# Kernel tuning notes

Measured on AMD Instinct MI355X. Metric: run time of the kernel, lower is better.

## Reference

```python
import jax, jax.numpy as jnp
import numpy as np

ALPHA = 0.2  # leaky_relu negative slope
NEG_INF = -9e15


def gat_layer(h_in, W, a, adj_mask):
    """One GATLayer (eval mode, dropout disabled).
    h_in: [N, F_in], W: [F_in, F_out], a: [2*F_out, 1], adj_mask: [N, N] bool.
    Equivalent to the torch repeat/cat construction: e_ij = leaky_relu(a1.h_i + a2.h_j).
    """
    h = h_in @ W                          # [N, F_out]
    F_out = W.shape[1]
    a1 = a[:F_out, 0]                     # [F_out]
    a2 = a[F_out:, 0]                     # [F_out]
    f1 = h @ a1                           # [N]
    f2 = h @ a2                           # [N]
    e = jax.nn.leaky_relu(f1[:, None] + f2[None, :], negative_slope=ALPHA)  # [N, N]
    e = jnp.where(adj_mask, e, NEG_INF)
    attn = jax.nn.softmax(e, axis=-1)     # rows sum to 1
    return jax.nn.elu(attn @ h)           # [N, F_out]


def setup_inputs() -> dict:
    key = jax.random.key(0)
    ks = jax.random.split(key, 6)
    N, F_in, F_hid, F_out, H = 8192, 29, 8, 2, 4
    x = jax.random.normal(ks[0], (N, F_in), dtype=jnp.float32)
    adj = jax.random.randint(ks[1], (N, N), 0, 2, dtype=jnp.int32)
    # xavier_uniform with gain=1.414
    def xavier(k, shape, gain=1.414):
        fan_in, fan_out = shape[0], shape[1]
        bound = gain * np.sqrt(6.0 / (fan_in + fan_out))
        return jax.random.uniform(k, shape, jnp.float32, -bound, bound)
    W_heads = jnp.stack([xavier(k, (F_in, F_hid)) for k in jax.random.split(ks[2], H)])   # [H, 29, 8]
    a_heads = jnp.stack([xavier(k, (2 * F_hid, 1)) for k in jax.random.split(ks[3], H)])  # [H, 16, 1]
    W_out = xavier(ks[4], (F_hid * H, F_out))   # [32, 2]
    a_out = xavier(ks[5], (2 * F_out, 1))       # [4, 1]
    return {"x": x, "adj": adj, "W_heads": W_heads, "a_heads": a_heads,
            "W_out": W_out, "a_out": a_out}


def reference(x, adj, W_heads, a_heads, W_out, a_out):
    adj_mask = adj > 0
    heads = jax.vmap(lambda W, a: gat_layer(x, W, a, adj_mask))(W_heads, a_heads)  # [H, N, 8]
    hcat = jnp.concatenate(list(heads), axis=1)   # [N, H*8] (same order as torch cat over heads)
    out = gat_layer(hcat, W_out, a_out, adj_mask)  # [N, 2]
    return jax.nn.log_softmax(out, axis=1)
```

## Files before the change

### kernel.cpp

```cpp
#include <hip/hip_runtime.h>
#include <math.h>

#define N 8192
#define FIN 29
#define FH 8
#define NH 4
#define ALPHA 0.2f
#define LOG2E 1.4426950408889634f
#define JS 8
#define JRR (N / JS)

typedef unsigned long long ull;
typedef unsigned short u16;
typedef __attribute__((ext_vector_type(8))) short bf16x8;
typedef __attribute__((ext_vector_type(4))) float f32x4;
typedef __attribute__((ext_vector_type(2))) float f32x2;

__device__ inline unsigned bf16rn(float f) {
    unsigned u = __float_as_uint(f);
    return (u + 0x7fffu + ((u >> 16) & 1u)) >> 16;
}
__device__ inline f32x2 pk_mul(f32x2 a, f32x2 b) {
    f32x2 d;
    asm("v_pk_mul_f32 %0, %1, %2" : "=v"(d) : "v"(a), "v"(b));
    return d;
}

#define WTILE(E1P2, E1N2, SW, ACC)                                              \
    {                                                                           \
        f32x2 wp, wn;                                                           \
        float w0, w1, w2, w3, w4, w5, w6, w7;                                   \
        wp = pk_mul(E1P2, p01); wn = pk_mul(E1N2, n01);                         \
        w0 = fmaxf(wp[0], wn[0]); w1 = fmaxf(wp[1], wn[1]);                     \
        wp = pk_mul(E1P2, p23); wn = pk_mul(E1N2, n23);                         \
        w2 = fmaxf(wp[0], wn[0]); w3 = fmaxf(wp[1], wn[1]);                     \
        wp = pk_mul(E1P2, p45); wn = pk_mul(E1N2, n45);                         \
        w4 = fmaxf(wp[0], wn[0]); w5 = fmaxf(wp[1], wn[1]);                     \
        wp = pk_mul(E1P2, p67); wn = pk_mul(E1N2, n67);                         \
        w6 = fmaxf(wp[0], wn[0]); w7 = fmaxf(wp[1], wn[1]);                     \
        w0 = (SW & 1u)   ? w0 : 0.f;                                            \
        w1 = (SW & 2u)   ? w1 : 0.f;                                            \
        w2 = (SW & 4u)   ? w2 : 0.f;                                            \
        w3 = (SW & 8u)   ? w3 : 0.f;                                            \
        w4 = (SW & 16u)  ? w4 : 0.f;                                            \
        w5 = (SW & 32u)  ? w5 : 0.f;                                            \
        w6 = (SW & 64u)  ? w6 : 0.f;                                            \
        w7 = (SW & 128u) ? w7 : 0.f;                                            \
        uint4 ap;                                                               \
        asm("v_cvt_pk_bf16_f32 %0, %1, %2" : "=v"(ap.x) : "v"(w0), "v"(w1));    \
        asm("v_cvt_pk_bf16_f32 %0, %1, %2" : "=v"(ap.y) : "v"(w2), "v"(w3));    \
        asm("v_cvt_pk_bf16_f32 %0, %1, %2" : "=v"(ap.z) : "v"(w4), "v"(w5));    \
        asm("v_cvt_pk_bf16_f32 %0, %1, %2" : "=v"(ap.w) : "v"(w6), "v"(w7));    \
        ACC = __builtin_amdgcn_mfma_f32_16x16x32_bf16(                          \
            __builtin_bit_cast(bf16x8, ap), __builtin_bit_cast(bf16x8, bp),     \
            ACC, 0, 0, 0);                                                      \
    }

__global__ void kPack(const int* __restrict__ adj, ull* __restrict__ maskT) {
    int row = blockIdx.x;
    int tid = threadIdx.x;
    int lane = tid & 63;
    int wv = tid >> 6;
    const int* rp = adj + (size_t)row * N;
#pragma unroll 8
    for (int i = 0; i < 32; i++) {
        int a = rp[i * 256 + tid];
        ull b = __ballot(a > 0);
        if (lane == 0) maskT[(size_t)(i * 4 + wv) * N + row] = b;
    }
}

__global__ __launch_bounds__(256) void kFeat(
    const float* __restrict__ x, const float* __restrict__ Wh,
    const float* __restrict__ ah,
    float* __restrict__ e2p, float* __restrict__ e2n, u16* __restrict__ Bpk,
    float* __restrict__ f1a, float* __restrict__ bmax1) {
    __shared__ float sx[64 * FIN];
    __shared__ float sW[NH * FIN * FH];
    __shared__ float sa[NH * 2 * FH];
    int tid = threadIdx.x;
    int wv = tid >> 6;
    for (int i = tid; i < NH * FIN * FH; i += 256) sW[i] = Wh[i];
    for (int i = tid; i < NH * 2 * FH; i += 256) sa[i] = ah[i];
    for (int i = tid; i < 64 * FIN; i += 256) sx[i] = x[(size_t)blockIdx.x * 64 * FIN + i];
    __syncthreads();
    int h = tid & 3;
    int nl = tid >> 2;
    int node = blockIdx.x * 64 + nl;
    float hv[FH];
#pragma unroll
    for (int k = 0; k < FH; k++) {
        float s = 0.f;
#pragma unroll
        for (int f = 0; f < FIN; f++) s += sx[nl * FIN + f] * sW[(h * FIN + f) * FH + k];
        hv[k] = s;
    }
    float f1 = 0.f, f2 = 0.f;
#pragma unroll
    for (int k = 0; k < FH; k++) {
        f1 += hv[k] * sa[h * 16 + k];
        f2 += hv[k] * sa[h * 16 + 8 + k];
    }
    float f1L = f1 * LOG2E, f2L = f2 * LOG2E;
    f1a[node * 4 + h] = f1L;
    e2p[(size_t)h * N + node] = __builtin_amdgcn_exp2f(f2L);
    e2n[(size_t)h * N + node] = __builtin_amdgcn_exp2f(ALPHA * f2L);
    int js = (node >> 10) & 7;
    int t  = (node >> 6) & 15;
    int hfl = (node >> 5) & 1;
    int kb = (node >> 3) & 3;
    int e  = node & 7;
    u16* dst = Bpk + ((size_t)(((h * 8 + js) * 16 + t) * 2 + hfl)) * 512 + e;
#pragma unroll
    for (int cc = 0; cc < 16; cc++) {
        u16 vv = (cc < FH) ? (u16)bf16rn(hv[cc])
                           : ((cc == 8) ? (u16)0x3F80u : (u16)0);
        dst[(kb * 16 + cc) * 8] = vv;
    }
    float v = f2L;
    for (int off = 4; off < 64; off <<= 1) v = fmaxf(v, __shfl_xor(v, off, 64));
    if ((tid & 63) < 4) bmax1[(tid & 3) * 512 + blockIdx.x * 4 + wv] = v;
}

__global__ __launch_bounds__(256, 6) void kB_attn1(
    const ull* __restrict__ maskT, const float* __restrict__ e2p,
    const float* __restrict__ e2n, const uint4* __restrict__ Bpk,
    const float* __restrict__ f1a, const float* __restrict__ bmax1,
    float* __restrict__ part1) {
    __shared__ __align__(16) float sE2p[JRR];
    __shared__ __align__(16) float sE2n[JRR];
    __shared__ float sred[4];
    int tid = threadIdx.x;
    int lane = tid & 63;
    int wv = tid >> 6;
    int h = blockIdx.x & 3;
    int js = (blockIdx.x >> 2) & 7;
    int rowblk = blockIdx.x >> 5;
    int jbase = js * JRR;

#pragma unroll
    for (int i = 0; i < JRR / 256; i++) {
        sE2p[tid + i * 256] = e2p[(size_t)h * N + jbase + tid + i * 256];
        sE2n[tid + i * 256] = e2n[(size_t)h * N + jbase + tid + i * 256];
    }
    float v = -3.0e38f;
    for (int i = tid; i < 512; i += 256) v = fmaxf(v, bmax1[h * 512 + i]);
    for (int off = 32; off > 0; off >>= 1) v = fmaxf(v, __shfl_xor(v, off, 64));
    if (lane == 0) sred[wv] = v;
    __syncthreads();
    float mfL = fmaxf(fmaxf(sred[0], sred[1]), fmaxf(sred[2], sred[3]));

    int c = lane & 15;
    int kb = lane >> 4;
    int sh = kb * 8;
    int r0 = rowblk * 128 + wv * 16 + c;
    int r1 = r0 + 64;

    float f1 = f1a[r0 * 4 + h];
    float vv = f1 + mfL, mm = fmaxf(vv, ALPHA * vv);
    f32x2 e1p0, e1n0, e1p1, e1n1;
    e1p0[0] = e1p0[1] = __builtin_amdgcn_exp2f(f1 - mm);
    e1n0[0] = e1n0[1] = __builtin_amdgcn_exp2f(ALPHA * f1 - mm);
    f1 = f1a[r1 * 4 + h];
    vv = f1 + mfL; mm = fmaxf(vv, ALPHA * vv);
    e1p1[0] = e1p1[1] = __builtin_amdgcn_exp2f(f1 - mm);
    e1n1[0] = e1n1[1] = __builtin_amdgcn_exp2f(ALPHA * f1 - mm);

    const ull* mT = maskT + (size_t)(js * (JRR / 64)) * N;
    const uint4* bp0 = Bpk + (size_t)(h * 8 + js) * 2048 + lane;
    const float* pph = sE2p + kb * 8;
    const float* nnh = sE2n + kb * 8;

    f32x4 acc0 = {0.f, 0.f, 0.f, 0.f};
    f32x4 acc1 = {0.f, 0.f, 0.f, 0.f};

    for (int t = 0; t < JRR / 64; t++) {
        ull mw0 = mT[(size_t)t * N + r0];
        ull mw1 = mT[(size_t)t * N + r1];
#pragma unroll
        for (int hf = 0; hf < 2; hf++) {
            f32x4 P0 = *(const f32x4*)(pph + t * 64 + hf * 32);
            f32x4 P1 = *(const f32x4*)(pph + t * 64 + hf * 32 + 4);
            f32x4 Q0 = *(const f32x4*)(nnh + t * 64 + hf * 32);
            f32x4 Q1 = *(const f32x4*)(nnh + t * 64 + hf * 32 + 4);
            f32x2 p01 = __builtin_shufflevector(P0, P0, 0, 1);
            f32x2 p23 = __builtin_shufflevector(P0, P0, 2, 3);
            f32x2 p45 = __builtin_shufflevector(P1, P1, 0, 1);
            f32x2 p67 = __builtin_shufflevector(P1, P1, 2, 3);
            f32x2 n01 = __builtin_shufflevector(Q0, Q0, 0, 1);
            f32x2 n23 = __builtin_shufflevector(Q0, Q0, 2, 3);
            f32x2 n45 = __builtin_shufflevector(Q1, Q1, 0, 1);
            f32x2 n67 = __builtin_shufflevector(Q1, Q1, 2, 3);
            uint4 bp = bp0[(t * 2 + hf) * 64];
            unsigned sw0 = ((unsigned)(mw0 >> (hf * 32))) >> sh;
            unsigned sw1 = ((unsigned)(mw1 >> (hf * 32))) >> sh;
            WTILE(e1p0, e1n0, sw0, acc0)
            WTILE(e1p1, e1n1, sw1, acc1)
        }
    }
    if (c <= 8) {
        int ro = rowblk * 128 + wv * 16 + kb * 4;
        float* dstp = part1 + (size_t)(js * 36 + h * 9 + c) * N + ro;
        *(float4*)dstp = make_float4(acc0[0], acc0[1], acc0[2], acc0[3]);
        *(float4*)(dstp + 64) = make_float4(acc1[0], acc1[1], acc1[2], acc1[3]);
    }
}

__global__ __launch_bounds__(64) void kC_final1(
    const float* __restrict__ part1, const float* __restrict__ Wo,
    const float* __restrict__ ao,
    float4* __restrict__ rec2, float* __restrict__ f1b,
    float* __restrict__ bmax2) {
    __shared__ float sW[64];
    __shared__ float sa[4];
    int tid = threadIdx.x;
    sW[tid] = Wo[tid];
    if (tid < 4) sa[tid] = ao[tid];
    __syncthreads();
    int row = blockIdx.x * 64 + tid;
    float hv[32];
#pragma unroll
    for (int h = 0; h < NH; h++) {
        float s[9];
#pragma unroll
        for (int cc = 0; cc < 9; cc++) {
            float acc = 0.f;
#pragma unroll
            for (int js = 0; js < JS; js++)
                acc += part1[(size_t)(js * 36 + h * 9 + cc) * N + row];
            s[cc] = acc;
        }
        float inv = 1.f / s[8];
#pragma unroll
        for (int k = 0; k < FH; k++) {
            float o = s[k] * inv;
            hv[h * 8 + k] = (o > 0.f) ? o : expm1f(o);
        }
    }
    float h0 = 0.f, h1 = 0.f;
#pragma unroll
    for (int i = 0; i < 32; i++) {
        h0 = fmaf(hv[i], sW[i * 2 + 0], h0);
        h1 = fmaf(hv[i], sW[i * 2 + 1], h1);
    }
    float f1 = (h0 * sa[0] + h1 * sa[1]) * LOG2E;
    float f2 = (h0 * sa[2] + h1 * sa[3]) * LOG2E;
    rec2[row] = make_float4(__builtin_amdgcn_exp2f(f2), h0, h1,
                            __builtin_amdgcn_exp2f(ALPHA * f2));
    f1b[row] = f1;
    float vmax = f2;
    for (int off = 32; off > 0; off >>= 1) vmax = fmaxf(vmax, __shfl_xor(vmax, off, 64));
    if (tid == 0) bmax2[blockIdx.x] = vmax;
}

__global__ __launch_bounds__(256) void kD_attn2(
    const ull* __restrict__ maskT, const float4* __restrict__ rec2,
    const float* __restrict__ f1b, const float* __restrict__ bmax2,
    float* __restrict__ out) {
    __shared__ float sred[4];
    int tid = threadIdx.x;
    int lane = tid & 63;
    int wv = tid >> 6;

    float v = (tid < 128) ? bmax2[tid] : -3.0e38f;
    for (int off = 32; off > 0; off >>= 1) v = fmaxf(v, __shfl_xor(v, off, 64));
    if (lane == 0) sred[wv] = v;
    __syncthreads();
    float mb = fmaxf(fmaxf(sred[0], sred[1]), fmaxf(sred[2], sred[3]));

    int r0 = blockIdx.x * 8 + wv * 2;
    float f1 = f1b[r0];
    float vv = f1 + mb, mm = fmaxf(vv, ALPHA * vv);
    float q1p0 = __builtin_amdgcn_exp2f(f1 - mm);
    float q1n0 = __builtin_amdgcn_exp2f(ALPHA * f1 - mm);
    f1 = f1b[r0 + 1];
    vv = f1 + mb; mm = fmaxf(vv, ALPHA * vv);
    float q1p1 = __builtin_amdgcn_exp2f(f1 - mm);
    float q1n1 = __builtin_amdgcn_exp2f(ALPHA * f1 - mm);

    float a00 = 0.f, a10 = 0.f, d0 = 0.f;
    float a01 = 0.f, a11 = 0.f, d1 = 0.f;
#pragma unroll 4
    for (int s = 0; s < N / 64; s++) {
        float4 q = rec2[s * 64 + lane];
        ull mw0 = maskT[(size_t)s * N + r0];
        ull mw1 = maskT[(size_t)s * N + r0 + 1];
        float w0 = fmaxf(q1p0 * q.x, q1n0 * q.w);
        w0 = ((mw0 >> lane) & 1ull) ? w0 : 0.f;
        float w1 = fmaxf(q1p1 * q.x, q1n1 * q.w);
        w1 = ((mw1 >> lane) & 1ull) ? w1 : 0.f;
        a00 = fmaf(w0, q.y, a00);
        a10 = fmaf(w0, q.z, a10);
        d0 += w0;
        a01 = fmaf(w1, q.y, a01);
        a11 = fmaf(w1, q.z, a11);
        d1 += w1;
    }
    for (int off = 32; off > 0; off >>= 1) {
        a00 += __shfl_xor(a00, off, 64);
        a10 += __shfl_xor(a10, off, 64);
        d0  += __shfl_xor(d0,  off, 64);
        a01 += __shfl_xor(a01, off, 64);
        a11 += __shfl_xor(a11, off, 64);
        d1  += __shfl_xor(d1,  off, 64);
    }
    if (lane == 0) {
#pragma unroll
        for (int i = 0; i < 2; i++) {
            float s0 = i ? a01 : a00;
            float s1 = i ? a11 : a10;
            float dd = i ? d1 : d0;
            float iv = 1.f / dd;
            float e0 = s0 * iv, e1 = s1 * iv;
            e0 = (e0 > 0.f) ? e0 : expm1f(e0);
            e1 = (e1 > 0.f) ? e1 : expm1f(e1);
            float mx = fmaxf(e0, e1);
            float lse = mx + logf(expf(e0 - mx) + expf(e1 - mx));
            ((float2*)out)[r0 + i] = make_float2(e0 - lse, e1 - lse);
        }
    }
}

extern "C" void kernel_launch(void* const* d_in, const int* in_sizes, int n_in,
                              void* d_out, int out_size, void* d_ws, size_t ws_size,
                              hipStream_t stream) {
    const float* x   = (const float*)d_in[0];
    const int*   adj = (const int*)d_in[1];
    const float* Wh  = (const float*)d_in[2];
    const float* ah  = (const float*)d_in[3];
    const float* Wo  = (const float*)d_in[4];
    const float* ao  = (const float*)d_in[5];
    float* out = (float*)d_out;
    float* ws = (float*)d_ws;

    ull*    maskT = (ull*)ws;
    float*  e2p   = ws + 2097152;
    float*  e2n   = ws + 2129920;
    u16*    Bpk   = (u16*)(ws + 2162688);
    float*  f1a   = ws + 2424832;
    float*  part1 = ws + 2457600;
    float4* rec2  = (float4*)(ws + 4816896);
    float*  f1b   = ws + 4849664;
    float*  bmax1 = ws + 4857856;
    float*  bmax2 = ws + 4859904;

    kPack<<<N, 256, 0, stream>>>(adj, maskT);
    kFeat<<<N / 64, 256, 0, stream>>>(x, Wh, ah, e2p, e2n, Bpk, f1a, bmax1);
    kB_attn1<<<(N / 128) * JS * NH, 256, 0, stream>>>(maskT, e2p, e2n,
                                                      (const uint4*)Bpk, f1a,
                                                      bmax1, part1);
    kC_final1<<<N / 64, 64, 0, stream>>>(part1, Wo, ao, rec2, f1b, bmax2);
    kD_attn2<<<N / 8, 256, 0, stream>>>(maskT, rec2, f1b, bmax2, out);
}
```

Baseline: 534.5 us.

## Merge pack and feature kernels, vectorize mask packing, prefetch attention loop loads

Fuses the adjacency bit-packing kernel and the feature kernel into one launch, with extra blocks doing the feature work, so one kernel launch goes away and the two jobs can overlap. Mask packing now reads int4 vectors and builds 64-bit words with shuffles instead of ballots. In the first attention kernel, the mask words and B-operand tiles for the next iteration are loaded before the current one is computed, which hides global load latency. The occupancy hint drops from 6 to 4 blocks to make room for the extra registers this needs.

```diff
diff --git a/kernel.cpp b/kernel.cpp
--- a/kernel.cpp
+++ b/kernel.cpp
@@ -26,7 +26,7 @@
     return d;
 }
 
-#define WTILE(E1P2, E1N2, SW, ACC)                                              \
+#define WTILE(E1P2, E1N2, SW, BP, ACC)                                          \
     {                                                                           \
         f32x2 wp, wn;                                                           \
         float w0, w1, w2, w3, w4, w5, w6, w7;                                   \
@@ -52,41 +52,53 @@
         asm("v_cvt_pk_bf16_f32 %0, %1, %2" : "=v"(ap.z) : "v"(w4), "v"(w5));    \
         asm("v_cvt_pk_bf16_f32 %0, %1, %2" : "=v"(ap.w) : "v"(w6), "v"(w7));    \
         ACC = __builtin_amdgcn_mfma_f32_16x16x32_bf16(                          \
-            __builtin_bit_cast(bf16x8, ap), __builtin_bit_cast(bf16x8, bp),     \
+            __builtin_bit_cast(bf16x8, ap), __builtin_bit_cast(bf16x8, BP),     \
             ACC, 0, 0, 0);                                                      \
     }
 
-__global__ void kPack(const int* __restrict__ adj, ull* __restrict__ maskT) {
-    int row = blockIdx.x;
-    int tid = threadIdx.x;
-    int lane = tid & 63;
-    int wv = tid >> 6;
-    const int* rp = adj + (size_t)row * N;
-#pragma unroll 8
-    for (int i = 0; i < 32; i++) {
-        int a = rp[i * 256 + tid];
-        ull b = __ballot(a > 0);
-        if (lane == 0) maskT[(size_t)(i * 4 + wv) * N + row] = b;
-    }
-}
-
-__global__ __launch_bounds__(256) void kFeat(
-    const float* __restrict__ x, const float* __restrict__ Wh,
-    const float* __restrict__ ah,
-    float* __restrict__ e2p, float* __restrict__ e2n, u16* __restrict__ Bpk,
-    float* __restrict__ f1a, float* __restrict__ bmax1) {
+__global__ __launch_bounds__(256) void kPF(
+    const int* __restrict__ adj, const float* __restrict__ x,
+    const float* __restrict__ Wh, const float* __restrict__ ah,
+    ull* __restrict__ maskT, float* __restrict__ e2p, float* __restrict__ e2n,
+    u16* __restrict__ Bpk, float* __restrict__ f1a, float* __restrict__ bmax1) {
+    const int tid = threadIdx.x;
+    const int blk = blockIdx.x;
+    const int lane = tid & 63;
+    const int wv = tid >> 6;
+
+    if (blk < N) {
+        int row = blk;
+        const int4* rp4 = (const int4*)(adj + (size_t)row * N);
+        int sub = (lane & 15) * 4;
+        int g = lane >> 4;
+#pragma unroll
+        for (int i = 0; i < 8; i++) {
+            int4 a = rp4[i * 256 + wv * 64 + lane];
+            unsigned n = (unsigned)(a.x > 0) | ((unsigned)(a.y > 0) << 1) |
+                         ((unsigned)(a.z > 0) << 2) | ((unsigned)(a.w > 0) << 3);
+            ull t = (ull)n << sub;
+            t |= __shfl_xor(t, 1, 64);
+            t |= __shfl_xor(t, 2, 64);
+            t |= __shfl_xor(t, 4, 64);
+            t |= __shfl_xor(t, 8, 64);
+            if ((lane & 15) == 0) {
+                int wglob = i * 16 + wv * 4 + g;
+                maskT[(size_t)wglob * N + row] = t;
+            }
+        }
+        return;
+    }
     __shared__ float sx[64 * FIN];
     __shared__ float sW[NH * FIN * FH];
     __shared__ float sa[NH * 2 * FH];
-    int tid = threadIdx.x;
-    int wv = tid >> 6;
+    int fb = blk - N;
     for (int i = tid; i < NH * FIN * FH; i += 256) sW[i] = Wh[i];
     for (int i = tid; i < NH * 2 * FH; i += 256) sa[i] = ah[i];
-    for (int i = tid; i < 64 * FIN; i += 256) sx[i] = x[(size_t)blockIdx.x * 64 * FIN + i];
+    for (int i = tid; i < 64 * FIN; i += 256) sx[i] = x[(size_t)fb * 64 * FIN + i];
     __syncthreads();
     int h = tid & 3;
     int nl = tid >> 2;
-    int node = blockIdx.x * 64 + nl;
+    int node = fb * 64 + nl;
     float hv[FH];
 #pragma unroll
     for (int k = 0; k < FH; k++) {
@@ -119,10 +131,10 @@
     }
     float v = f2L;
     for (int off = 4; off < 64; off <<= 1) v = fmaxf(v, __shfl_xor(v, off, 64));
-    if ((tid & 63) < 4) bmax1[(tid & 3) * 512 + blockIdx.x * 4 + wv] = v;
-}
-
-__global__ __launch_bounds__(256, 6) void kB_attn1(
+    if ((tid & 63) < 4) bmax1[(tid & 3) * 512 + fb * 4 + wv] = v;
+}
+
+__global__ __launch_bounds__(256, 4) void kB_attn1(
     const ull* __restrict__ maskT, const float* __restrict__ e2p,
     const float* __restrict__ e2n, const uint4* __restrict__ Bpk,
     const float* __restrict__ f1a, const float* __restrict__ bmax1,
@@ -166,7 +178,8 @@
     e1p1[0] = e1p1[1] = __builtin_amdgcn_exp2f(f1 - mm);
     e1n1[0] = e1n1[1] = __builtin_amdgcn_exp2f(ALPHA * f1 - mm);
 
-    const ull* mT = maskT + (size_t)(js * (JRR / 64)) * N;
+    const ull* mrow0 = maskT + (size_t)(js * (JRR / 64)) * N + r0;
+    const ull* mrow1 = maskT + (size_t)(js * (JRR / 64)) * N + r1;
     const uint4* bp0 = Bpk + (size_t)(h * 8 + js) * 2048 + lane;
     const float* pph = sE2p + kb * 8;
     const float* nnh = sE2n + kb * 8;
@@ -174,9 +187,20 @@
     f32x4 acc0 = {0.f, 0.f, 0.f, 0.f};
     f32x4 acc1 = {0.f, 0.f, 0.f, 0.f};
 
+    ull mw0 = mrow0[0];
+    ull mw1 = mrow1[0];
+    uint4 bpA = bp0[0];
+    uint4 bpB = bp0[64];
+
     for (int t = 0; t < JRR / 64; t++) {
-        ull mw0 = mT[(size_t)t * N + r0];
-        ull mw1 = mT[(size_t)t * N + r1];
+        ull nmw0 = mw0, nmw1 = mw1;
+        uint4 nbpA = bpA, nbpB = bpB;
+        if (t < JRR / 64 - 1) {
+            nmw0 = mrow0[(size_t)(t + 1) * N];
+            nmw1 = mrow1[(size_t)(t + 1) * N];
+            nbpA = bp0[(t + 1) * 128];
+            nbpB = bp0[(t + 1) * 128 + 64];
+        }
 #pragma unroll
         for (int hf = 0; hf < 2; hf++) {
             f32x4 P0 = *(const f32x4*)(pph + t * 64 + hf * 32);
@@ -191,12 +215,13 @@
             f32x2 n23 = __builtin_shufflevector(Q0, Q0, 2, 3);
             f32x2 n45 = __builtin_shufflevector(Q1, Q1, 0, 1);
             f32x2 n67 = __builtin_shufflevector(Q1, Q1, 2, 3);
-            uint4 bp = bp0[(t * 2 + hf) * 64];
+            uint4 bp = hf ? bpB : bpA;
             unsigned sw0 = ((unsigned)(mw0 >> (hf * 32))) >> sh;
             unsigned sw1 = ((unsigned)(mw1 >> (hf * 32))) >> sh;
-            WTILE(e1p0, e1n0, sw0, acc0)
-            WTILE(e1p1, e1n1, sw1, acc1)
-        }
+            WTILE(e1p0, e1n0, sw0, bp, acc0)
+            WTILE(e1p1, e1n1, sw1, bp, acc1)
+        }
+        mw0 = nmw0; mw1 = nmw1; bpA = nbpA; bpB = nbpB;
     }
     if (c <= 8) {
         int ro = rowblk * 128 + wv * 16 + kb * 4;
@@ -344,8 +369,8 @@
     float*  bmax1 = ws + 4857856;
     float*  bmax2 = ws + 4859904;
 
-    kPack<<<N, 256, 0, stream>>>(adj, maskT);
-    kFeat<<<N / 64, 256, 0, stream>>>(x, Wh, ah, e2p, e2n, Bpk, f1a, bmax1);
+    kPF<<<N + 128, 256, 0, stream>>>(adj, x, Wh, ah, maskT, e2p, e2n, Bpk,
+                                     f1a, bmax1);
     kB_attn1<<<(N / 128) * JS * NH, 256, 0, stream>>>(maskT, e2p, e2n,
                                                       (const uint4*)Bpk, f1a,
                                                       bmax1, part1);
```

Result: faster. 506.1 us (-5.3%).
